# Kernel optimization log

Hardware: AMD Instinct MI355X
Metric: run time of the kernel (lower is better)

Reference implementation:

```python
import jax, jax.numpy as jnp
import numpy as np

WINDOW = (2, 6, 12)  # (Wz, Wh, Ww), N = 144
HEADS = 6
TYPE_OF_WINDOWS = 10


def _position_index(ws):
    Wz, Wh, Ww = ws
    zi = np.arange(Wz); zj = -np.arange(Wz) * Wz
    hi = np.arange(Wh); hj = -np.arange(Wh) * Wh
    w = np.arange(Ww)
    c1 = np.stack(np.meshgrid(zi, hi, w, indexing='ij')).reshape(3, -1)
    c2 = np.stack(np.meshgrid(zj, hj, w, indexing='ij')).reshape(3, -1)
    coords = (c1[:, :, None] - c2[:, None, :]).transpose(1, 2, 0).copy()
    coords[:, :, 2] += Ww - 1
    coords[:, :, 1] *= 2 * Ww - 1
    coords[:, :, 0] *= (2 * Ww - 1) * Wh * Wh
    return coords.sum(-1).reshape(-1)  # [N*N]


def setup_inputs() -> dict:
    key = jax.random.key(0)
    ks = jax.random.split(key, 7)
    B, nW, C = 96, TYPE_OF_WINDOWS, 192
    N = WINDOW[0] * WINDOW[1] * WINDOW[2]
    bias_len = (2 * WINDOW[2] - 1) * WINDOW[1] ** 2 * WINDOW[0] ** 2
    return {
        'x': jax.random.normal(ks[0], (B, nW, N, C), jnp.float32),
        'mask': jax.random.normal(ks[1], (B, N, N), jnp.float32),
        'w_qkv': jax.random.normal(ks[2], (C, 3 * C), jnp.float32) * 0.02,
        'b_qkv': jnp.zeros((3 * C,), jnp.float32),
        'w_proj': jax.random.normal(ks[3], (C, C), jnp.float32) * 0.02,
        'b_proj': jnp.zeros((C,), jnp.float32),
        'bias_table': jax.random.normal(ks[4], (bias_len, nW, HEADS), jnp.float32) * 0.02,
        'position_index': jnp.asarray(_position_index(WINDOW), jnp.int32),
    }


def reference(x, mask, w_qkv, b_qkv, w_proj, b_proj, bias_table, position_index):
    B, nW, N, C = x.shape
    H = HEADS
    Dh = C // H
    scale = Dh ** -0.5
    qkv = x @ w_qkv + b_qkv                       # [B,nW,N,3C]
    qkv = qkv.reshape(B, nW, N, 3, H, Dh)
    qkv = qkv.transpose(3, 0, 1, 4, 2, 5)         # [3,B,nW,H,N,Dh]
    q, k, v = qkv[0], qkv[1], qkv[2]
    attn = jnp.einsum('bwhnd,bwhmd->bwhnm', q * scale, k)   # [B,nW,H,N,N]
    bias = bias_table[position_index]             # [N*N,nW,H]
    bias = bias.reshape(N, N, nW, H).transpose(2, 3, 0, 1)  # [nW,H,N,N]
    attn = attn + bias[None] + mask[:, None, None, :, :]
    attn = jax.nn.softmax(attn, axis=-1)
    out = jnp.einsum('bwhnm,bwhmd->bwhnd', attn, v)         # [B,nW,H,N,Dh]
    out = out.transpose(0, 1, 3, 2, 4).reshape(B, nW, N, C)
    return out @ w_proj + b_proj
```

## Files before the change

### kernel.cpp

```cpp
#include <hip/hip_runtime.h>
#include <math.h>

#define B_   96
#define NW   10
#define NN   144
#define CC   192
#define HH   6
#define DH   32
#define SCALE 0.17677669529663687f

#define XP 200
#define PP 152
#define NPASS 3
#define BWCHUNK 320
#define QKV_STRIDE (NN * DH)

typedef __attribute__((ext_vector_type(8))) short v8s;
typedef __attribute__((ext_vector_type(4))) unsigned short v4us;
typedef __attribute__((ext_vector_type(4))) float v4f;

__device__ __forceinline__ unsigned short f2b(float f) {
  union { float f; unsigned u; } v; v.f = f;
  unsigned r = v.u + 0x7fffu + ((v.u >> 16) & 1u);
  return (unsigned short)(r >> 16);
}
__device__ __forceinline__ float b2f(unsigned short s) {
  union { unsigned u; float f; } v; v.u = ((unsigned)s) << 16;
  return v.f;
}

#define N_WQT (576*192)
#define N_WPT (192*192)
#define N_BIAS (NW*HH*NN*NN)

__global__ __launch_bounds__(256) void prep_kernel(
    const float* __restrict__ w_qkv, const float* __restrict__ w_proj,
    const float* __restrict__ bias_table, const int* __restrict__ pos,
    unsigned short* __restrict__ wqT, unsigned short* __restrict__ wpT,
    unsigned short* __restrict__ biasNN)
{
  int i = blockIdx.x * 256 + threadIdx.x;
  if (i < N_WQT) {
    int n = i / 192, k = i % 192;
    wqT[i] = f2b(w_qkv[k * 576 + n]);
  } else if (i < N_WQT + N_WPT) {
    int j = i - N_WQT;
    int n = j / 192, k = j % 192;
    wpT[j] = f2b(w_proj[k * 192 + n]);
  } else if (i < N_WQT + N_WPT + N_BIAS) {
    int j = i - (N_WQT + N_WPT);
    int m = j % NN, n = (j / NN) % NN, h = (j / (NN * NN)) % HH, w = j / (NN * NN * HH);
    biasNN[j] = f2b(bias_table[(pos[n * NN + m] * NW + w) * HH + h]);
  }
}

__global__ __launch_bounds__(256, 3) void qkv_gemm(
    const float* __restrict__ x, const float* __restrict__ b_qkv,
    const unsigned short* __restrict__ wqT,
    unsigned short* __restrict__ qkv, int bw0)
{
  __shared__ unsigned short xs[48 * XP];
  const int tid  = threadIdx.x;
  const int wave = tid >> 6, lane = tid & 63;
  const int lr = lane & 15, lk8 = (lane >> 4) * 8, quad = lane >> 4;
  const int bwl = blockIdx.x / 3;
  const int rt3 = blockIdx.x % 3;
  const int bw  = bw0 + bwl;

  const float4* xp4 = (const float4*)(x + ((size_t)bw * NN + rt3 * 48) * CC);
  for (int i = tid; i < 48 * (CC / 4); i += 256) {
    float4 f = xp4[i];
    int r = i / (CC / 4), c = (i % (CC / 4)) * 4;
    unsigned short* d = &xs[r * XP + c];
    d[0] = f2b(f.x); d[1] = f2b(f.y); d[2] = f2b(f.z); d[3] = f2b(f.w);
  }
  __syncthreads();

  v8s a[3][6];
  #pragma unroll
  for (int ii = 0; ii < 3; ii++)
    #pragma unroll
    for (int ks = 0; ks < 6; ks++)
      a[ii][ks] = *(const v8s*)&xs[(ii * 16 + lr) * XP + ks * 32 + lk8];

  for (int c = wave; c < 36; c += 4) {
    const int s = c / 12;
    const int h = (c % 12) >> 1;
    const int dhalf = c & 1;
    const unsigned short* wrow = wqT + (size_t)(c * 16 + lr) * CC;
    v8s bf[6];
    #pragma unroll
    for (int ks = 0; ks < 6; ks++) bf[ks] = *(const v8s*)&wrow[ks * 32 + lk8];
    const float bv = b_qkv[c * 16 + lr];
    v4f acc[3];
    #pragma unroll
    for (int ii = 0; ii < 3; ii++) acc[ii] = (v4f){bv, bv, bv, bv};
    #pragma unroll
    for (int ks = 0; ks < 6; ks++)
      #pragma unroll
      for (int ii = 0; ii < 3; ii++)
        acc[ii] = __builtin_amdgcn_mfma_f32_16x16x32_bf16(a[ii][ks], bf[ks], acc[ii], 0, 0, 0);

    if (s == 2) {
      unsigned short* opT = qkv + ((size_t)(bwl * HH + h) * 3 + 2) * QKV_STRIDE
                          + (size_t)(dhalf * 16 + lr) * NN;
      #pragma unroll
      for (int ii = 0; ii < 3; ii++) {
        const int n0 = rt3 * 48 + ii * 16 + quad * 4;
        v4us pk;
        #pragma unroll
        for (int r = 0; r < 4; r++) pk[r] = f2b(acc[ii][r]);
        *(v4us*)&opT[n0] = pk;
      }
    } else {
      unsigned short* op = qkv + ((size_t)(bwl * HH + h) * 3 + s) * QKV_STRIDE + dhalf * 16 + lr;
      #pragma unroll
      for (int ii = 0; ii < 3; ii++)
        #pragma unroll
        for (int r = 0; r < 4; r++) {
          const int n = rt3 * 48 + ii * 16 + quad * 4 + r;
          op[n * DH] = f2b(acc[ii][r]);
        }
    }
  }
}

__global__ __launch_bounds__(256, 2) void attn_bwh(
    const unsigned short* __restrict__ qkv, const float* __restrict__ mask,
    const unsigned short* __restrict__ biasNN,
    unsigned short* __restrict__ ao, int bw0)
{
  __shared__ unsigned short Ps[NN * PP];

  const int tid  = threadIdx.x;
  const int wave = tid >> 6, lane = tid & 63;
  const int lr = lane & 15, lk8 = (lane >> 4) * 8, quad = lane >> 4;

  const int bwl = blockIdx.x / HH;
  const int h   = blockIdx.x % HH;
  const int bw  = bw0 + bwl;
  const int b   = bw / NW;
  const int w   = bw % NW;

  const unsigned short* qp = qkv + (size_t)(bwl * HH + h) * 3 * QKV_STRIDE;
  const unsigned short* kp = qp + QKV_STRIDE;
  const unsigned short* vT = qp + 2 * QKV_STRIDE;

  v8s bv[2][4], bvt[2];
  #pragma unroll
  for (int dh2 = 0; dh2 < 2; dh2++) {
    const unsigned short* vrow = vT + (size_t)(dh2 * 16 + lr) * NN;
    #pragma unroll
    for (int ks = 0; ks < 4; ks++) bv[dh2][ks] = *(const v8s*)&vrow[ks * 32 + lk8];
    bvt[dh2] = *(const v8s*)&vrow[128 + (lk8 & 8)];
  }

  v8s aq[9];
  #pragma unroll
  for (int nt = 0; nt < 9; nt++)
    aq[nt] = *(const v8s*)&qp[(nt * 16 + lr) * DH + lk8];

  for (int mt = wave; mt < 9; mt += 4) {
    v8s bk = *(const v8s*)&kp[(mt * 16 + lr) * DH + lk8];
    const int m = mt * 16 + lr;
    #pragma unroll
    for (int nt = 0; nt < 9; nt++) {
      v4f c = {0.f, 0.f, 0.f, 0.f};
      c = __builtin_amdgcn_mfma_f32_16x16x32_bf16(aq[nt], bk, c, 0, 0, 0);
      #pragma unroll
      for (int r = 0; r < 4; r++) {
        const int n = nt * 16 + quad * 4 + r;
        Ps[n * PP + m] = f2b(c[r] * SCALE);
      }
    }
  }
  __syncthreads();

  const unsigned short* bp = biasNN + (size_t)(w * HH + h) * NN * NN;
  const float* mp = mask + (size_t)b * NN * NN;
  for (int rr = 0; rr < 9; rr++) {
    const int row = rr * 16 + wave * 4 + quad;
    unsigned short* prow = &Ps[row * PP];
    const unsigned short* brow = bp + (size_t)row * NN;
    const float* mrow = mp + (size_t)row * NN;
    float bm[9];
    #pragma unroll
    for (int j = 0; j < 9; j++)
      bm[j] = b2f(brow[j * 16 + lr]) + mrow[j * 16 + lr];
    float e[9];
    float mx = -1e30f;
    #pragma unroll
    for (int j = 0; j < 9; j++) {
      e[j] = b2f(prow[j * 16 + lr]) + bm[j];
      mx = fmaxf(mx, e[j]);
    }
    #pragma unroll
    for (int off = 8; off; off >>= 1) mx = fmaxf(mx, __shfl_xor(mx, off, 64));
    float s = 0.f;
    #pragma unroll
    for (int j = 0; j < 9; j++) { e[j] = __expf(e[j] - mx); s += e[j]; }
    #pragma unroll
    for (int off = 8; off; off >>= 1) s += __shfl_xor(s, off, 64);
    const float inv = 1.f / s;
    #pragma unroll
    for (int j = 0; j < 9; j++) prow[j * 16 + lr] = f2b(e[j] * inv);
  }
  __syncthreads();

  const v8s vzero = {};
  for (int nt = wave; nt < 9; nt += 4) {
    v8s ap[4];
    #pragma unroll
    for (int ks = 0; ks < 4; ks++)
      ap[ks] = *(const v8s*)&Ps[(nt * 16 + lr) * PP + ks * 32 + lk8];
    v8s at = *(const v8s*)&Ps[(nt * 16 + lr) * PP + 128 + (lk8 & 8)];
    at = (quad < 2) ? at : vzero;
    #pragma unroll
    for (int dh2 = 0; dh2 < 2; dh2++) {
      v4f c = {0.f, 0.f, 0.f, 0.f};
      #pragma unroll
      for (int ks = 0; ks < 4; ks++)
        c = __builtin_amdgcn_mfma_f32_16x16x32_bf16(ap[ks], bv[dh2][ks], c, 0, 0, 0);
      c = __builtin_amdgcn_mfma_f32_16x16x32_bf16(at, bvt[dh2], c, 0, 0, 0);
      #pragma unroll
      for (int r = 0; r < 4; r++) {
        const int n = nt * 16 + quad * 4 + r;
        ao[((size_t)bw * NN + n) * CC + h * DH + dh2 * 16 + lr] = f2b(c[r]);
      }
    }
  }
}

__global__ __launch_bounds__(256) void proj_mfma(
    const unsigned short* __restrict__ ao,
    const unsigned short* __restrict__ wpT,
    const float* __restrict__ b_proj,
    float* __restrict__ out)
{
  __shared__ unsigned short As[64 * XP];
  const int tid  = threadIdx.x;
  const int wave = tid >> 6, lane = tid & 63;
  const int lr = lane & 15, lk8 = (lane >> 4) * 8, quad = lane >> 4;
  const size_t row0 = (size_t)blockIdx.x * 64;

  for (int i = tid; i < 64 * 24; i += 256) {
    const int r = i / 24, c = i % 24;
    *(v8s*)&As[r * XP + c * 8] = *(const v8s*)(ao + (row0 + r) * CC + c * 8);
  }
  __syncthreads();

  v4f acc[12];
  #pragma unroll
  for (int j = 0; j < 12; j++) {
    const float bv = b_proj[j * 16 + lr];
    acc[j] = (v4f){bv, bv, bv, bv};
  }
  #pragma unroll
  for (int ks = 0; ks < 6; ks++) {
    const int k0 = ks * 32;
    v8s a = *(const v8s*)&As[(wave * 16 + lr) * XP + k0 + lk8];
    #pragma unroll
    for (int j = 0; j < 12; j++) {
      v8s bf = *(const v8s*)(wpT + (j * 16 + lr) * CC + k0 + lk8);
      acc[j] = __builtin_amdgcn_mfma_f32_16x16x32_bf16(a, bf, acc[j], 0, 0, 0);
    }
  }
  #pragma unroll
  for (int j = 0; j < 12; j++)
    #pragma unroll
    for (int r = 0; r < 4; r++)
      out[(row0 + wave * 16 + quad * 4 + r) * CC + j * 16 + lr] = acc[j][r];
}

extern "C" void kernel_launch(void* const* d_in, const int* in_sizes, int n_in,
                              void* d_out, int out_size, void* d_ws, size_t ws_size,
                              hipStream_t stream)
{
  const float* x          = (const float*)d_in[0];
  const float* mask       = (const float*)d_in[1];
  const float* w_qkv      = (const float*)d_in[2];
  const float* b_qkv      = (const float*)d_in[3];
  const float* w_proj     = (const float*)d_in[4];
  const float* b_proj     = (const float*)d_in[5];
  const float* bias_table = (const float*)d_in[6];
  const int*   pos        = (const int*)d_in[7];
  float* out = (float*)d_out;

  unsigned short* biasNN = (unsigned short*)d_ws;
  unsigned short* wqT    = biasNN + N_BIAS;
  unsigned short* wpT    = wqT + N_WQT;
  unsigned short* qkvws  = wpT + N_WPT;
  unsigned short* ao     = qkvws + (size_t)BWCHUNK * HH * 3 * QKV_STRIDE;

  const int prep_total = N_WQT + N_WPT + N_BIAS;
  prep_kernel<<<(prep_total + 255) / 256, 256, 0, stream>>>(
      w_qkv, w_proj, bias_table, pos, wqT, wpT, biasNN);

  for (int p = 0; p < NPASS; p++) {
    const int bw0 = p * BWCHUNK;
    qkv_gemm<<<BWCHUNK * 3, 256, 0, stream>>>(x, b_qkv, wqT, qkvws, bw0);
    attn_bwh<<<BWCHUNK * HH, 256, 0, stream>>>(qkvws, mask, biasNN, ao, bw0);
  }
  proj_mfma<<<(B_ * NW * NN) / 64, 256, 0, stream>>>(ao, wpT, b_proj, out);
}
```

Before: 513.4 us.

## Restructure proj GEMM to keep weight fragments in registers per wave

```diff
diff --git a/kernel.cpp b/kernel.cpp
--- a/kernel.cpp
+++ b/kernel.cpp
@@ -237,39 +237,44 @@
     const float* __restrict__ b_proj,
     float* __restrict__ out)
 {
-  __shared__ unsigned short As[64 * XP];
   const int tid  = threadIdx.x;
   const int wave = tid >> 6, lane = tid & 63;
   const int lr = lane & 15, lk8 = (lane >> 4) * 8, quad = lane >> 4;
   const size_t row0 = (size_t)blockIdx.x * 64;
-
-  for (int i = tid; i < 64 * 24; i += 256) {
-    const int r = i / 24, c = i % 24;
-    *(v8s*)&As[r * XP + c * 8] = *(const v8s*)(ao + (row0 + r) * CC + c * 8);
-  }
-  __syncthreads();
-
-  v4f acc[12];
-  #pragma unroll
-  for (int j = 0; j < 12; j++) {
-    const float bv = b_proj[j * 16 + lr];
-    acc[j] = (v4f){bv, bv, bv, bv};
-  }
-  #pragma unroll
-  for (int ks = 0; ks < 6; ks++) {
-    const int k0 = ks * 32;
-    v8s a = *(const v8s*)&As[(wave * 16 + lr) * XP + k0 + lk8];
-    #pragma unroll
-    for (int j = 0; j < 12; j++) {
-      v8s bf = *(const v8s*)(wpT + (j * 16 + lr) * CC + k0 + lk8);
-      acc[j] = __builtin_amdgcn_mfma_f32_16x16x32_bf16(a, bf, acc[j], 0, 0, 0);
-    }
-  }
-  #pragma unroll
-  for (int j = 0; j < 12; j++)
-    #pragma unroll
-    for (int r = 0; r < 4; r++)
-      out[(row0 + wave * 16 + quad * 4 + r) * CC + j * 16 + lr] = acc[j][r];
+  const int j0 = wave * 3;
+
+  v8s bf[3][6];
+  #pragma unroll
+  for (int jj = 0; jj < 3; jj++)
+    #pragma unroll
+    for (int ks = 0; ks < 6; ks++)
+      bf[jj][ks] = *(const v8s*)(wpT + (size_t)((j0 + jj) * 16 + lr) * CC + ks * 32 + lk8);
+
+  float bvj[3];
+  #pragma unroll
+  for (int jj = 0; jj < 3; jj++) bvj[jj] = b_proj[(j0 + jj) * 16 + lr];
+
+  #pragma unroll
+  for (int rt = 0; rt < 4; rt++) {
+    const size_t r0 = row0 + rt * 16;
+    v8s a[6];
+    #pragma unroll
+    for (int ks = 0; ks < 6; ks++)
+      a[ks] = *(const v8s*)(ao + (r0 + lr) * CC + ks * 32 + lk8);
+    v4f acc[3];
+    #pragma unroll
+    for (int jj = 0; jj < 3; jj++) acc[jj] = (v4f){bvj[jj], bvj[jj], bvj[jj], bvj[jj]};
+    #pragma unroll
+    for (int ks = 0; ks < 6; ks++)
+      #pragma unroll
+      for (int jj = 0; jj < 3; jj++)
+        acc[jj] = __builtin_amdgcn_mfma_f32_16x16x32_bf16(a[ks], bf[jj][ks], acc[jj], 0, 0, 0);
+    #pragma unroll
+    for (int jj = 0; jj < 3; jj++)
+      #pragma unroll
+      for (int r = 0; r < 4; r++)
+        out[(r0 + quad * 4 + r) * CC + (j0 + jj) * 16 + lr] = acc[jj][r];
+  }
 }
 
 extern "C" void kernel_launch(void* const* d_in, const int* in_sizes, int n_in,
```

Result: faster. 476.1 us (-7.3%).
